# Performance work log

Measured on AMD Instinct MI355X. Metric: run time of the kernel, lower is better.

Reference implementation:

```python
import jax, jax.numpy as jnp
import numpy as np

N, T, H, O, S, R = 64, 1024, 256, 80, 128, 2


def _lin(k, fin, fout):
    kw, kb = jax.random.split(k)
    s = 1.0 / np.sqrt(fin)
    return (jax.random.uniform(kw, (fout, fin), jnp.float32, -s, s),
            jax.random.uniform(kb, (fout,), jnp.float32, -s, s))


def _gru_params(k, fin, hid):
    k1, k2, k3, k4 = jax.random.split(k, 4)
    s = 1.0 / np.sqrt(hid)
    u = lambda kk, shp: jax.random.uniform(kk, shp, jnp.float32, -s, s)
    return u(k1, (3 * hid, fin)), u(k2, (3 * hid, hid)), u(k3, (3 * hid,)), u(k4, (3 * hid,))


def setup_inputs() -> dict:
    key = jax.random.key(0)
    ks = jax.random.split(key, 16)
    inp = {}
    inp["input_enc"] = jax.random.normal(ks[0], (N, T, 2 * H), jnp.float32)
    inp["input_attW_enc"] = jax.random.normal(ks[1], (N, T, 2 * H), jnp.float32)
    inp["input_dec"] = jax.random.normal(ks[2], (N, O), jnp.float32)
    inp["style_vec"] = jax.random.normal(ks[3], (N, 1, S), jnp.float32)
    lengths = jnp.sort(jax.random.randint(ks[4], (N,), 1, T + 1))[::-1]
    inp["lengths_enc"] = lengths.at[0].set(T)  # pack_padded requires max(len)==T, descending
    inp["pw1"], inp["pb1"] = _lin(ks[5], O, 2 * H)
    inp["pw2"], inp["pb2"] = _lin(ks[6], 2 * H, H)
    inp["wdec"], inp["bdec"] = _lin(ks[7], 2 * H, 2 * H)
    inp["ga_ih"], inp["ga_hh"], inp["ga_bih"], inp["ga_bhh"] = _gru_params(ks[8], 3 * H + S, 2 * H)
    inp["wattn"], inp["battn"] = _lin(ks[9], 2 * H, 1)
    inp["wsc"], inp["bsc"] = _lin(ks[10], 4 * H + S, 2 * H)
    inp["g1_ih"], inp["g1_hh"], inp["g1_bih"], inp["g1_bhh"] = _gru_params(ks[11], 4 * H + S, 2 * H)
    inp["g2_ih"], inp["g2_hh"], inp["g2_bih"], inp["g2_bhh"] = _gru_params(ks[12], 2 * H, 2 * H)
    inp["wout"], inp["bout"] = _lin(ks[13], 2 * H, R * O)
    return inp


def _gru_cell(x, h, w_ih, w_hh, b_ih, b_hh):
    # PyTorch GRU cell: gates order (r, z, n)
    gi = x @ w_ih.T + b_ih
    gh = h @ w_hh.T + b_hh
    ir, iz, inn = jnp.split(gi, 3, -1)
    hr, hz, hn = jnp.split(gh, 3, -1)
    r = jax.nn.sigmoid(ir + hr)
    z = jax.nn.sigmoid(iz + hz)
    n = jnp.tanh(inn + r * hn)
    return (1.0 - z) * n + z * h


def reference(input_enc, input_attW_enc, input_dec, style_vec,
              pw1, pb1, pw2, pb2, wdec, bdec,
              ga_ih, ga_hh, ga_bih, ga_bhh,
              wattn, battn, wsc, bsc,
              g1_ih, g1_hh, g1_bih, g1_bhh,
              g2_ih, g2_hh, g2_bih, g2_bhh,
              wout, bout, lengths_enc):
    Nn, Tt, D2 = input_enc.shape
    Hh = D2 // 2
    # prenet (dropout disabled: eval-mode reference)
    pre = jax.nn.relu(jax.nn.relu(input_dec @ pw1.T + pb1) @ pw2.T + pb2)  # (N,H)
    ctx0 = jnp.zeros((Nn, 2 * Hh), input_enc.dtype)  # input_context=None -> zeros
    sv = style_vec[:, 0, :]
    x_att = jnp.concatenate([pre, ctx0, sv], axis=-1)  # (N,3H+S)
    h0 = jnp.zeros((Nn, 2 * Hh), input_enc.dtype)  # hidden states start None -> zeros
    out_att = _gru_cell(x_att, h0, ga_ih, ga_hh, ga_bih, ga_bhh)  # (N,2H)
    attW_dec = out_att @ wdec.T + bdec  # (N,2H), broadcast over T (expand_as)
    e = jnp.tanh(input_attW_enc + attW_dec[:, None, :])  # (N,T,2H)
    score = e @ wattn.T + battn  # (N,T,1)
    mask = (jnp.arange(Tt)[None, :] < lengths_enc[:, None]).astype(score.dtype)[..., None]
    w = jnp.exp(score) * mask  # pack/pad zeroes padded positions
    w = w / jnp.maximum(jnp.sum(w, axis=1, keepdims=True), 1e-12)  # F.normalize(p=1, dim=1)
    attn_applied = jnp.einsum('nt,ntd->nd', w[..., 0], input_enc)  # bmm(w^T, enc) -> (N,2H)
    out_dec = jnp.concatenate([attn_applied, out_att, sv], axis=-1)  # (N,4H+S)
    residual = out_dec @ wsc.T + bsc
    h1 = _gru_cell(out_dec, h0, g1_ih, g1_hh, g1_bih, g1_bhh)
    residual = residual + h1
    h2 = _gru_cell(residual, h0, g2_ih, g2_hh, g2_bih, g2_bhh)
    residual = residual + h2
    output = (residual @ wout.T + bout).reshape(Nn, R, -1)  # (N,r,O)
    return output, attn_applied[:, None, :]
```

## Files before the change

### kernel.cpp

```cpp
#include <hip/hip_runtime.h>
#include <math.h>

#define NB  64
#define TT  1024
#define H2  512
#define SS  128
#define OO  80
#define FIN_A 896
#define FIN_1 1152
#define CH  32

__device__ __forceinline__ float fast_rcp(float x) { return __builtin_amdgcn_rcpf(x); }
__device__ __forceinline__ float fast_sigmoid(float x) { return fast_rcp(1.0f + __expf(-x)); }
__device__ __forceinline__ float fast_tanh(float x) {
    float e = __expf(2.0f * x);
    return 1.0f - 2.0f * fast_rcp(e + 1.0f);
}
__device__ __forceinline__ float wred(float p) {
    #pragma unroll
    for (int o = 32; o > 0; o >>= 1) p += __shfl_xor(p, o, 64);
    return p;
}

__global__ void k_l1(const float* __restrict__ xdec, const float* __restrict__ pw1,
                     const float* __restrict__ pb1, const float* __restrict__ sv,
                     float* __restrict__ t1T, float* __restrict__ xaT,
                     float* __restrict__ out_decT) {
    int wv = threadIdx.x >> 6, lane = threadIdx.x & 63;
    if (blockIdx.x < 128) {
        int i = blockIdx.x * 4 + wv;
        const float* w = pw1 + i * OO;
        const float* x = xdec + lane * OO;
        float acc = 0.0f;
        #pragma unroll 8
        for (int k = 0; k < OO; ++k) acc += w[k] * x[k];
        t1T[i * 64 + lane] = fmaxf(acc + pb1[i], 0.0f);
    } else {
        int s = (blockIdx.x - 128) * 4 + wv;
        float v = sv[lane * SS + s];
        xaT[(256 + s) * 64 + lane] = v;
        out_decT[(1024 + s) * 64 + lane] = v;
    }
}

__global__ void k_l2(const float* __restrict__ t1T, const float* __restrict__ pw2,
                     const float* __restrict__ pb2, float* __restrict__ xaT) {
    int i = blockIdx.x;
    int wv = threadIdx.x >> 6, lane = threadIdx.x & 63;
    int k0 = wv * 128;
    const float* w = pw2 + (size_t)i * H2 + k0;
    const float* xT = t1T + k0 * 64;
    float p = 0.0f;
    #pragma unroll 8
    for (int k = 0; k < 128; ++k) p += w[k] * xT[k * 64 + lane];
    __shared__ float s[4][64];
    s[wv][lane] = p;
    __syncthreads();
    if (wv == 0) {
        float acc = s[0][lane] + s[1][lane] + s[2][lane] + s[3][lane];
        xaT[i * 64 + lane] = fmaxf(acc + pb2[i], 0.0f);
    }
}

__global__ void k_gruA(const float* __restrict__ xaT, const float* __restrict__ ga_ih,
                       const float* __restrict__ ga_bih, const float* __restrict__ ga_bhh,
                       float* __restrict__ out_decT) {
    int j = blockIdx.x;
    int wv = threadIdx.x >> 6, lane = threadIdx.x & 63;
    int k0 = wv * 96;
    const float* wr = ga_ih + (size_t)j * FIN_A;
    const float* wz = ga_ih + (size_t)(H2 + j) * FIN_A;
    const float* wn = ga_ih + (size_t)(2 * H2 + j) * FIN_A;
    float pr = 0.0f, pz = 0.0f, pn = 0.0f;
    #pragma unroll 8
    for (int kk = 0; kk < 96; ++kk) {
        int k = k0 + kk;
        int wc = k + (k >= 256 ? 512 : 0);
        float xv = xaT[k * 64 + lane];
        pr += wr[wc] * xv; pz += wz[wc] * xv; pn += wn[wc] * xv;
    }
    __shared__ float s[3][4][64];
    s[0][wv][lane] = pr; s[1][wv][lane] = pz; s[2][wv][lane] = pn;
    __syncthreads();
    if (wv == 0) {
        float fr = s[0][0][lane] + s[0][1][lane] + s[0][2][lane] + s[0][3][lane];
        float fz = s[1][0][lane] + s[1][1][lane] + s[1][2][lane] + s[1][3][lane];
        float fn = s[2][0][lane] + s[2][1][lane] + s[2][2][lane] + s[2][3][lane];
        float r = fast_sigmoid(fr + ga_bih[j] + ga_bhh[j]);
        float z = fast_sigmoid(fz + ga_bih[H2 + j] + ga_bhh[H2 + j]);
        float nn = fast_tanh(fn + ga_bih[2 * H2 + j] + r * ga_bhh[2 * H2 + j]);
        out_decT[(H2 + j) * 64 + lane] = (1.0f - z) * nn;
    }
}

__global__ void k_attw(const float* __restrict__ out_decT, const float* __restrict__ wdec,
                       const float* __restrict__ bdec, float* __restrict__ attW_dec) {
    int i = blockIdx.x;
    int wv = threadIdx.x >> 6, lane = threadIdx.x & 63;
    int k0 = wv * 128;
    const float* w = wdec + (size_t)i * H2 + k0;
    const float* xT = out_decT + (H2 + k0) * 64;
    float p = 0.0f;
    #pragma unroll 8
    for (int k = 0; k < 128; ++k) p += w[k] * xT[k * 64 + lane];
    __shared__ float s[4][64];
    s[wv][lane] = p;
    __syncthreads();
    if (wv == 0) {
        float acc = s[0][lane] + s[1][lane] + s[2][lane] + s[3][lane];
        attW_dec[lane * H2 + i] = acc + bdec[i];
    }
}

__global__ void k_score(const float* __restrict__ attw_enc, const float* __restrict__ attW_dec,
                        const float* __restrict__ wattn, const float* __restrict__ battn,
                        const int* __restrict__ lengths, float* __restrict__ ew) {
    int wv = threadIdx.x >> 6, lane = threadIdx.x & 63;
    int row = blockIdx.x * 4 + wv;
    int n = row >> 10, t = row & 1023;
    if (t >= lengths[n]) { if (lane == 0) ew[row] = 0.0f; return; }
    const float4* e4 = (const float4*)(attw_enc + (size_t)row * H2);
    const float4* d4 = (const float4*)(attW_dec + n * H2);
    const float4* w4 = (const float4*)wattn;
    float p = 0.0f;
    #pragma unroll
    for (int m = 0; m < 2; ++m) {
        int idx = lane + m * 64;
        float4 e = e4[idx], d = d4[idx], w = w4[idx];
        p += fast_tanh(e.x + d.x) * w.x + fast_tanh(e.y + d.y) * w.y +
             fast_tanh(e.z + d.z) * w.z + fast_tanh(e.w + d.w) * w.w;
    }
    p = wred(p);
    if (lane == 0) ew[row] = __expf(p + battn[0]);
}

__global__ void k_apply(const float* __restrict__ enc, const float* __restrict__ ew,
                        float* __restrict__ num_part ,
                        float* __restrict__ den_part ) {
    int n = blockIdx.y, c = blockIdx.x;
    int wv = threadIdx.x >> 6, lane = threadIdx.x & 63;
    int t0 = c * (TT / CH) + wv * (TT / CH / 4);
    int d0 = lane * 8;
    const float* base = enc + ((size_t)n * TT + t0) * H2 + d0;
    const float* ewp = ew + n * TT + t0;
    float4 a0 = {0, 0, 0, 0}, a1 = {0, 0, 0, 0};
    float dp = 0.0f;
    #pragma unroll
    for (int t = 0; t < TT / CH / 4; ++t) {
        float wt = ewp[t];
        if (wt != 0.0f) {
            const float4* v4 = (const float4*)(base + (size_t)t * H2);
            float4 v0 = v4[0], v1 = v4[1];
            a0.x += wt * v0.x; a0.y += wt * v0.y; a0.z += wt * v0.z; a0.w += wt * v0.w;
            a1.x += wt * v1.x; a1.y += wt * v1.y; a1.z += wt * v1.z; a1.w += wt * v1.w;
            dp += wt;
        }
    }
    __shared__ float s[4 * 512];
    __shared__ float sd[4];
    float4* srow = (float4*)(s + wv * 512 + d0);
    srow[0] = a0; srow[1] = a1;
    if (lane == 0) sd[wv] = dp;
    __syncthreads();
    int d = threadIdx.x;
    float r0 = s[d] + s[512 + d] + s[1024 + d] + s[1536 + d];
    float r1 = s[256 + d] + s[768 + d] + s[1280 + d] + s[1792 + d];
    num_part[((size_t)c * H2 + d) * 64 + n] = r0;
    num_part[((size_t)c * H2 + 256 + d) * 64 + n] = r1;
    if (threadIdx.x == 0) den_part[c * NB + n] = sd[0] + sd[1] + sd[2] + sd[3];
}

__global__ void k_reduce(const float* __restrict__ num_part, const float* __restrict__ den_part,
                         float* __restrict__ out, float* __restrict__ out_decT) {
    int d = blockIdx.x * 4 + (threadIdx.x >> 6);
    int lane = threadIdx.x & 63;
    float s = 0.0f, den = 0.0f;
    #pragma unroll 8
    for (int c = 0; c < CH; ++c) {
        s += num_part[((size_t)c * H2 + d) * 64 + lane];
        den += den_part[c * NB + lane];
    }
    float a = s / fmaxf(den, 1e-12f);
    out_decT[d * 64 + lane] = a;
    out[NB * 160 + lane * H2 + d] = a;
}

__global__ void k_sc_h1(const float* __restrict__ out_decT, const float* __restrict__ wsc,
                        const float* __restrict__ bsc, const float* __restrict__ g1_ih,
                        const float* __restrict__ g1_bih, const float* __restrict__ g1_bhh,
                        float* __restrict__ res1T) {
    int j = blockIdx.x;
    int wv = threadIdx.x >> 6, lane = threadIdx.x & 63;
    int k0 = wv * 288;
    const float* ws_ = wsc + (size_t)j * FIN_1 + k0;
    const float* wr = g1_ih + (size_t)j * FIN_1 + k0;
    const float* wz = g1_ih + (size_t)(H2 + j) * FIN_1 + k0;
    const float* wn = g1_ih + (size_t)(2 * H2 + j) * FIN_1 + k0;
    const float* xT = out_decT + k0 * 64;
    float ps = 0.0f, pr = 0.0f, pz = 0.0f, pn = 0.0f;
    #pragma unroll 8
    for (int k = 0; k < 288; ++k) {
        float xv = xT[k * 64 + lane];
        ps += ws_[k] * xv; pr += wr[k] * xv; pz += wz[k] * xv; pn += wn[k] * xv;
    }
    __shared__ float s[4][4][64];
    s[0][wv][lane] = ps; s[1][wv][lane] = pr; s[2][wv][lane] = pz; s[3][wv][lane] = pn;
    __syncthreads();
    if (wv == 0) {
        float fs = s[0][0][lane] + s[0][1][lane] + s[0][2][lane] + s[0][3][lane];
        float fr = s[1][0][lane] + s[1][1][lane] + s[1][2][lane] + s[1][3][lane];
        float fz = s[2][0][lane] + s[2][1][lane] + s[2][2][lane] + s[2][3][lane];
        float fn = s[3][0][lane] + s[3][1][lane] + s[3][2][lane] + s[3][3][lane];
        float r = fast_sigmoid(fr + g1_bih[j] + g1_bhh[j]);
        float z = fast_sigmoid(fz + g1_bih[H2 + j] + g1_bhh[H2 + j]);
        float nn = fast_tanh(fn + g1_bih[2 * H2 + j] + r * g1_bhh[2 * H2 + j]);
        res1T[j * 64 + lane] = fs + bsc[j] + (1.0f - z) * nn;
    }
}

__global__ void k_h2(const float* __restrict__ res1T, const float* __restrict__ g2_ih,
                     const float* __restrict__ g2_bih, const float* __restrict__ g2_bhh,
                     float* __restrict__ res2T) {
    int j = blockIdx.x;
    int wv = threadIdx.x >> 6, lane = threadIdx.x & 63;
    int k0 = wv * 128;
    const float* wr = g2_ih + (size_t)j * H2 + k0;
    const float* wz = g2_ih + (size_t)(H2 + j) * H2 + k0;
    const float* wn = g2_ih + (size_t)(2 * H2 + j) * H2 + k0;
    const float* xT = res1T + k0 * 64;
    float pr = 0.0f, pz = 0.0f, pn = 0.0f;
    #pragma unroll 8
    for (int k = 0; k < 128; ++k) {
        float xv = xT[k * 64 + lane];
        pr += wr[k] * xv; pz += wz[k] * xv; pn += wn[k] * xv;
    }
    __shared__ float s[3][4][64];
    s[0][wv][lane] = pr; s[1][wv][lane] = pz; s[2][wv][lane] = pn;
    __syncthreads();
    if (wv == 0) {
        float fr = s[0][0][lane] + s[0][1][lane] + s[0][2][lane] + s[0][3][lane];
        float fz = s[1][0][lane] + s[1][1][lane] + s[1][2][lane] + s[1][3][lane];
        float fn = s[2][0][lane] + s[2][1][lane] + s[2][2][lane] + s[2][3][lane];
        float r = fast_sigmoid(fr + g2_bih[j] + g2_bhh[j]);
        float z = fast_sigmoid(fz + g2_bih[H2 + j] + g2_bhh[H2 + j]);
        float nn = fast_tanh(fn + g2_bih[2 * H2 + j] + r * g2_bhh[2 * H2 + j]);
        res2T[j * 64 + lane] = res1T[j * 64 + lane] + (1.0f - z) * nn;
    }
}

__global__ void k_out(const float* __restrict__ res2T, const float* __restrict__ wout,
                      const float* __restrict__ bout, float* __restrict__ out) {
    int i = blockIdx.x;
    int wv = threadIdx.x >> 6, lane = threadIdx.x & 63;
    int k0 = wv * 128;
    const float* w = wout + (size_t)i * H2 + k0;
    const float* xT = res2T + k0 * 64;
    float p = 0.0f;
    #pragma unroll 8
    for (int k = 0; k < 128; ++k) p += w[k] * xT[k * 64 + lane];
    __shared__ float s[4][64];
    s[wv][lane] = p;
    __syncthreads();
    if (wv == 0) {
        float acc = s[0][lane] + s[1][lane] + s[2][lane] + s[3][lane];
        out[lane * 160 + i] = acc + bout[i];
    }
}

extern "C" void kernel_launch(void* const* d_in, const int* in_sizes, int n_in,
                              void* d_out, int out_size, void* d_ws, size_t ws_size,
                              hipStream_t stream) {
    const float* input_enc      = (const float*)d_in[0];
    const float* input_attW_enc = (const float*)d_in[1];
    const float* input_dec      = (const float*)d_in[2];
    const float* style_vec      = (const float*)d_in[3];
    const int*   lengths_enc    = (const int*)d_in[4];
    const float* pw1  = (const float*)d_in[5];
    const float* pb1  = (const float*)d_in[6];
    const float* pw2  = (const float*)d_in[7];
    const float* pb2  = (const float*)d_in[8];
    const float* wdec = (const float*)d_in[9];
    const float* bdec = (const float*)d_in[10];
    const float* ga_ih  = (const float*)d_in[11];
    const float* ga_bih = (const float*)d_in[13];
    const float* ga_bhh = (const float*)d_in[14];
    const float* wattn  = (const float*)d_in[15];
    const float* battn  = (const float*)d_in[16];
    const float* wsc    = (const float*)d_in[17];
    const float* bsc    = (const float*)d_in[18];
    const float* g1_ih  = (const float*)d_in[19];
    const float* g1_bih = (const float*)d_in[21];
    const float* g1_bhh = (const float*)d_in[22];
    const float* g2_ih  = (const float*)d_in[23];
    const float* g2_bih = (const float*)d_in[25];
    const float* g2_bhh = (const float*)d_in[26];
    const float* wout   = (const float*)d_in[27];
    const float* bout   = (const float*)d_in[28];
    float* out = (float*)d_out;

    float* ws = (float*)d_ws;
    float* num_part = ws;
    float* den_part = ws + 1048576;
    float* t1T      = ws + 1050624;
    float* xaT      = ws + 1083392;
    float* out_decT = ws + 1107968;
    float* attW_dec = ws + 1181696;
    float* ew       = ws + 1214464;
    float* res1T    = ws + 1280000;
    float* res2T    = ws + 1312768;

    k_l1<<<160, 256, 0, stream>>>(input_dec, pw1, pb1, style_vec, t1T, xaT, out_decT);
    k_l2<<<256, 256, 0, stream>>>(t1T, pw2, pb2, xaT);
    k_gruA<<<512, 256, 0, stream>>>(xaT, ga_ih, ga_bih, ga_bhh, out_decT);
    k_attw<<<512, 256, 0, stream>>>(out_decT, wdec, bdec, attW_dec);
    k_score<<<NB * TT / 4, 256, 0, stream>>>(input_attW_enc, attW_dec, wattn, battn,
                                             lengths_enc, ew);
    k_apply<<<dim3(CH, NB), 256, 0, stream>>>(input_enc, ew, num_part, den_part);
    k_reduce<<<128, 256, 0, stream>>>(num_part, den_part, out, out_decT);
    k_sc_h1<<<512, 256, 0, stream>>>(out_decT, wsc, bsc, g1_ih, g1_bih, g1_bhh, res1T);
    k_h2<<<512, 256, 0, stream>>>(res1T, g2_ih, g2_bih, g2_bhh, res2T);
    k_out<<<160, 256, 0, stream>>>(res2T, wout, bout, out);
}
```

Baseline: 401.1 us.

## Fuse attention score into apply kernel and widen GEMV blocks to eight waves

Merges the score kernel into the attention-apply kernel. Each block computes exp-scores for its 32 timesteps into shared memory before the weighted sum, so the global ew buffer and one launch go away. It also doubles the waves per block in the small GEMV/GRU kernels so the K dimension is split eight ways, and k_sc_h1 uses float2 weight loads. The risk is that the fused kernel serialises score and apply work inside each block, with less parallelism in the score phase than the old 16K-block launch.

```diff
diff --git a/kernel.cpp b/kernel.cpp
--- a/kernel.cpp
+++ b/kernel.cpp
@@ -43,49 +43,55 @@
     }
 }
 
-__global__ void k_l2(const float* __restrict__ t1T, const float* __restrict__ pw2,
-                     const float* __restrict__ pb2, float* __restrict__ xaT) {
+__global__ __launch_bounds__(512) void k_l2(const float* __restrict__ t1T,
+                                            const float* __restrict__ pw2,
+                                            const float* __restrict__ pb2,
+                                            float* __restrict__ xaT) {
     int i = blockIdx.x;
     int wv = threadIdx.x >> 6, lane = threadIdx.x & 63;
-    int k0 = wv * 128;
+    int k0 = wv * 64;
     const float* w = pw2 + (size_t)i * H2 + k0;
     const float* xT = t1T + k0 * 64;
     float p = 0.0f;
     #pragma unroll 8
-    for (int k = 0; k < 128; ++k) p += w[k] * xT[k * 64 + lane];
-    __shared__ float s[4][64];
+    for (int k = 0; k < 64; ++k) p += w[k] * xT[k * 64 + lane];
+    __shared__ float s[8][64];
     s[wv][lane] = p;
     __syncthreads();
     if (wv == 0) {
-        float acc = s[0][lane] + s[1][lane] + s[2][lane] + s[3][lane];
+        float acc = 0.0f;
+        #pragma unroll
+        for (int q = 0; q < 8; ++q) acc += s[q][lane];
         xaT[i * 64 + lane] = fmaxf(acc + pb2[i], 0.0f);
     }
 }
 
-__global__ void k_gruA(const float* __restrict__ xaT, const float* __restrict__ ga_ih,
-                       const float* __restrict__ ga_bih, const float* __restrict__ ga_bhh,
-                       float* __restrict__ out_decT) {
+__global__ __launch_bounds__(512) void k_gruA(const float* __restrict__ xaT,
+                                              const float* __restrict__ ga_ih,
+                                              const float* __restrict__ ga_bih,
+                                              const float* __restrict__ ga_bhh,
+                                              float* __restrict__ out_decT) {
     int j = blockIdx.x;
     int wv = threadIdx.x >> 6, lane = threadIdx.x & 63;
-    int k0 = wv * 96;
+    int k0 = wv * 48;
     const float* wr = ga_ih + (size_t)j * FIN_A;
     const float* wz = ga_ih + (size_t)(H2 + j) * FIN_A;
     const float* wn = ga_ih + (size_t)(2 * H2 + j) * FIN_A;
     float pr = 0.0f, pz = 0.0f, pn = 0.0f;
     #pragma unroll 8
-    for (int kk = 0; kk < 96; ++kk) {
+    for (int kk = 0; kk < 48; ++kk) {
         int k = k0 + kk;
         int wc = k + (k >= 256 ? 512 : 0);
         float xv = xaT[k * 64 + lane];
         pr += wr[wc] * xv; pz += wz[wc] * xv; pn += wn[wc] * xv;
     }
-    __shared__ float s[3][4][64];
+    __shared__ float s[3][8][64];
     s[0][wv][lane] = pr; s[1][wv][lane] = pz; s[2][wv][lane] = pn;
     __syncthreads();
     if (wv == 0) {
-        float fr = s[0][0][lane] + s[0][1][lane] + s[0][2][lane] + s[0][3][lane];
-        float fz = s[1][0][lane] + s[1][1][lane] + s[1][2][lane] + s[1][3][lane];
-        float fn = s[2][0][lane] + s[2][1][lane] + s[2][2][lane] + s[2][3][lane];
+        float fr = 0.0f, fz = 0.0f, fn = 0.0f;
+        #pragma unroll
+        for (int q = 0; q < 8; ++q) { fr += s[0][q][lane]; fz += s[1][q][lane]; fn += s[2][q][lane]; }
         float r = fast_sigmoid(fr + ga_bih[j] + ga_bhh[j]);
         float z = fast_sigmoid(fz + ga_bih[H2 + j] + ga_bhh[H2 + j]);
         float nn = fast_tanh(fn + ga_bih[2 * H2 + j] + r * ga_bhh[2 * H2 + j]);
@@ -93,71 +99,84 @@
     }
 }
 
-__global__ void k_attw(const float* __restrict__ out_decT, const float* __restrict__ wdec,
-                       const float* __restrict__ bdec, float* __restrict__ attW_dec) {
+__global__ __launch_bounds__(512) void k_attw(const float* __restrict__ out_decT,
+                                              const float* __restrict__ wdec,
+                                              const float* __restrict__ bdec,
+                                              float* __restrict__ attW_dec) {
     int i = blockIdx.x;
     int wv = threadIdx.x >> 6, lane = threadIdx.x & 63;
-    int k0 = wv * 128;
+    int k0 = wv * 64;
     const float* w = wdec + (size_t)i * H2 + k0;
     const float* xT = out_decT + (H2 + k0) * 64;
     float p = 0.0f;
     #pragma unroll 8
-    for (int k = 0; k < 128; ++k) p += w[k] * xT[k * 64 + lane];
-    __shared__ float s[4][64];
+    for (int k = 0; k < 64; ++k) p += w[k] * xT[k * 64 + lane];
+    __shared__ float s[8][64];
     s[wv][lane] = p;
     __syncthreads();
     if (wv == 0) {
-        float acc = s[0][lane] + s[1][lane] + s[2][lane] + s[3][lane];
+        float acc = 0.0f;
+        #pragma unroll
+        for (int q = 0; q < 8; ++q) acc += s[q][lane];
         attW_dec[lane * H2 + i] = acc + bdec[i];
     }
 }
 
-__global__ void k_score(const float* __restrict__ attw_enc, const float* __restrict__ attW_dec,
-                        const float* __restrict__ wattn, const float* __restrict__ battn,
-                        const int* __restrict__ lengths, float* __restrict__ ew) {
-    int wv = threadIdx.x >> 6, lane = threadIdx.x & 63;
-    int row = blockIdx.x * 4 + wv;
-    int n = row >> 10, t = row & 1023;
-    if (t >= lengths[n]) { if (lane == 0) ew[row] = 0.0f; return; }
-    const float4* e4 = (const float4*)(attw_enc + (size_t)row * H2);
-    const float4* d4 = (const float4*)(attW_dec + n * H2);
-    const float4* w4 = (const float4*)wattn;
-    float p = 0.0f;
-    #pragma unroll
-    for (int m = 0; m < 2; ++m) {
-        int idx = lane + m * 64;
-        float4 e = e4[idx], d = d4[idx], w = w4[idx];
-        p += fast_tanh(e.x + d.x) * w.x + fast_tanh(e.y + d.y) * w.y +
-             fast_tanh(e.z + d.z) * w.z + fast_tanh(e.w + d.w) * w.w;
-    }
-    p = wred(p);
-    if (lane == 0) ew[row] = __expf(p + battn[0]);
-}
-
-__global__ void k_apply(const float* __restrict__ enc, const float* __restrict__ ew,
-                        float* __restrict__ num_part ,
-                        float* __restrict__ den_part ) {
+__global__ __launch_bounds__(256, 8) void k_attn(
+        const float* __restrict__ enc, const float* __restrict__ attw_enc,
+        const float* __restrict__ attW_dec, const float* __restrict__ wattn,
+        const float* __restrict__ battn, const int* __restrict__ lengths,
+        float* __restrict__ num_part ,
+        float* __restrict__ den_part ) {
     int n = blockIdx.y, c = blockIdx.x;
     int wv = threadIdx.x >> 6, lane = threadIdx.x & 63;
-    int t0 = c * (TT / CH) + wv * (TT / CH / 4);
+    int t0 = c * (TT / CH);
+    int len = lengths[n];
+    __shared__ float sew[TT / CH];
+    __shared__ float s[4 * 512];
+    __shared__ float sd[4];
+
+    {
+        const float4* d4 = (const float4*)(attW_dec + n * H2);
+        const float4* w4 = (const float4*)wattn;
+        float b = battn[0];
+        #pragma unroll
+        for (int r = 0; r < 8; ++r) {
+            int t = t0 + wv * 8 + r;
+            float val = 0.0f;
+            if (t < len) {
+                const float4* e4 = (const float4*)(attw_enc + ((size_t)(n * TT + t)) * H2);
+                float p = 0.0f;
+                #pragma unroll
+                for (int m = 0; m < 2; ++m) {
+                    int idx = lane + m * 64;
+                    float4 e = e4[idx], d = d4[idx], w = w4[idx];
+                    p += fast_tanh(e.x + d.x) * w.x + fast_tanh(e.y + d.y) * w.y +
+                         fast_tanh(e.z + d.z) * w.z + fast_tanh(e.w + d.w) * w.w;
+                }
+                p = wred(p);
+                val = __expf(p + b);
+            }
+            if (lane == 0) sew[wv * 8 + r] = val;
+        }
+    }
+    __syncthreads();
+
     int d0 = lane * 8;
-    const float* base = enc + ((size_t)n * TT + t0) * H2 + d0;
-    const float* ewp = ew + n * TT + t0;
+    const float* base = enc + ((size_t)(n * TT + t0 + wv * 8)) * H2 + d0;
     float4 a0 = {0, 0, 0, 0}, a1 = {0, 0, 0, 0};
     float dp = 0.0f;
     #pragma unroll
-    for (int t = 0; t < TT / CH / 4; ++t) {
-        float wt = ewp[t];
+    for (int r = 0; r < 8; ++r) {
+        float wt = sew[wv * 8 + r];
         if (wt != 0.0f) {
-            const float4* v4 = (const float4*)(base + (size_t)t * H2);
+            const float4* v4 = (const float4*)(base + (size_t)r * H2);
             float4 v0 = v4[0], v1 = v4[1];
             a0.x += wt * v0.x; a0.y += wt * v0.y; a0.z += wt * v0.z; a0.w += wt * v0.w;
             a1.x += wt * v1.x; a1.y += wt * v1.y; a1.z += wt * v1.z; a1.w += wt * v1.w;
             dp += wt;
         }
     }
-    __shared__ float s[4 * 512];
-    __shared__ float sd[4];
     float4* srow = (float4*)(s + wv * 512 + d0);
     srow[0] = a0; srow[1] = a1;
     if (lane == 0) sd[wv] = dp;
@@ -185,32 +204,46 @@
     out[NB * 160 + lane * H2 + d] = a;
 }
 
-__global__ void k_sc_h1(const float* __restrict__ out_decT, const float* __restrict__ wsc,
-                        const float* __restrict__ bsc, const float* __restrict__ g1_ih,
-                        const float* __restrict__ g1_bih, const float* __restrict__ g1_bhh,
-                        float* __restrict__ res1T) {
+__global__ __launch_bounds__(512) void k_sc_h1(const float* __restrict__ out_decT,
+                                               const float* __restrict__ wsc,
+                                               const float* __restrict__ bsc,
+                                               const float* __restrict__ g1_ih,
+                                               const float* __restrict__ g1_bih,
+                                               const float* __restrict__ g1_bhh,
+                                               float* __restrict__ res1T) {
     int j = blockIdx.x;
     int wv = threadIdx.x >> 6, lane = threadIdx.x & 63;
-    int k0 = wv * 288;
+    int k0 = wv * 144;
     const float* ws_ = wsc + (size_t)j * FIN_1 + k0;
     const float* wr = g1_ih + (size_t)j * FIN_1 + k0;
     const float* wz = g1_ih + (size_t)(H2 + j) * FIN_1 + k0;
     const float* wn = g1_ih + (size_t)(2 * H2 + j) * FIN_1 + k0;
     const float* xT = out_decT + k0 * 64;
-    float ps = 0.0f, pr = 0.0f, pz = 0.0f, pn = 0.0f;
-    #pragma unroll 8
-    for (int k = 0; k < 288; ++k) {
-        float xv = xT[k * 64 + lane];
-        ps += ws_[k] * xv; pr += wr[k] * xv; pz += wz[k] * xv; pn += wn[k] * xv;
-    }
-    __shared__ float s[4][4][64];
-    s[0][wv][lane] = ps; s[1][wv][lane] = pr; s[2][wv][lane] = pz; s[3][wv][lane] = pn;
-    __syncthreads();
-    if (wv == 0) {
-        float fs = s[0][0][lane] + s[0][1][lane] + s[0][2][lane] + s[0][3][lane];
-        float fr = s[1][0][lane] + s[1][1][lane] + s[1][2][lane] + s[1][3][lane];
-        float fz = s[2][0][lane] + s[2][1][lane] + s[2][2][lane] + s[2][3][lane];
-        float fn = s[3][0][lane] + s[3][1][lane] + s[3][2][lane] + s[3][3][lane];
+    float2 ps = {0, 0}, pr = {0, 0}, pz = {0, 0}, pn = {0, 0};
+    #pragma unroll 4
+    for (int k = 0; k < 144; k += 2) {
+        float x0 = xT[k * 64 + lane];
+        float x1 = xT[(k + 1) * 64 + lane];
+        float2 a = *(const float2*)(ws_ + k);
+        float2 b = *(const float2*)(wr + k);
+        float2 cc = *(const float2*)(wz + k);
+        float2 dd = *(const float2*)(wn + k);
+        ps.x += a.x * x0; ps.y += a.y * x1;
+        pr.x += b.x * x0; pr.y += b.y * x1;
+        pz.x += cc.x * x0; pz.y += cc.y * x1;
+        pn.x += dd.x * x0; pn.y += dd.y * x1;
+    }
+    __shared__ float s[4][8][64];
+    s[0][wv][lane] = ps.x + ps.y; s[1][wv][lane] = pr.x + pr.y;
+    s[2][wv][lane] = pz.x + pz.y; s[3][wv][lane] = pn.x + pn.y;
+    __syncthreads();
+    if (wv == 0) {
+        float fs = 0.0f, fr = 0.0f, fz = 0.0f, fn = 0.0f;
+        #pragma unroll
+        for (int q = 0; q < 8; ++q) {
+            fs += s[0][q][lane]; fr += s[1][q][lane];
+            fz += s[2][q][lane]; fn += s[3][q][lane];
+        }
         float r = fast_sigmoid(fr + g1_bih[j] + g1_bhh[j]);
         float z = fast_sigmoid(fz + g1_bih[H2 + j] + g1_bhh[H2 + j]);
         float nn = fast_tanh(fn + g1_bih[2 * H2 + j] + r * g1_bhh[2 * H2 + j]);
@@ -218,29 +251,31 @@
     }
 }
 
-__global__ void k_h2(const float* __restrict__ res1T, const float* __restrict__ g2_ih,
-                     const float* __restrict__ g2_bih, const float* __restrict__ g2_bhh,
-                     float* __restrict__ res2T) {
+__global__ __launch_bounds__(512) void k_h2(const float* __restrict__ res1T,
+                                            const float* __restrict__ g2_ih,
+                                            const float* __restrict__ g2_bih,
+                                            const float* __restrict__ g2_bhh,
+                                            float* __restrict__ res2T) {
     int j = blockIdx.x;
     int wv = threadIdx.x >> 6, lane = threadIdx.x & 63;
-    int k0 = wv * 128;
+    int k0 = wv * 64;
     const float* wr = g2_ih + (size_t)j * H2 + k0;
     const float* wz = g2_ih + (size_t)(H2 + j) * H2 + k0;
     const float* wn = g2_ih + (size_t)(2 * H2 + j) * H2 + k0;
     const float* xT = res1T + k0 * 64;
     float pr = 0.0f, pz = 0.0f, pn = 0.0f;
     #pragma unroll 8
-    for (int k = 0; k < 128; ++k) {
+    for (int k = 0; k < 64; ++k) {
         float xv = xT[k * 64 + lane];
         pr += wr[k] * xv; pz += wz[k] * xv; pn += wn[k] * xv;
     }
-    __shared__ float s[3][4][64];
+    __shared__ float s[3][8][64];
     s[0][wv][lane] = pr; s[1][wv][lane] = pz; s[2][wv][lane] = pn;
     __syncthreads();
     if (wv == 0) {
-        float fr = s[0][0][lane] + s[0][1][lane] + s[0][2][lane] + s[0][3][lane];
-        float fz = s[1][0][lane] + s[1][1][lane] + s[1][2][lane] + s[1][3][lane];
-        float fn = s[2][0][lane] + s[2][1][lane] + s[2][2][lane] + s[2][3][lane];
+        float fr = 0.0f, fz = 0.0f, fn = 0.0f;
+        #pragma unroll
+        for (int q = 0; q < 8; ++q) { fr += s[0][q][lane]; fz += s[1][q][lane]; fn += s[2][q][lane]; }
         float r = fast_sigmoid(fr + g2_bih[j] + g2_bhh[j]);
         float z = fast_sigmoid(fz + g2_bih[H2 + j] + g2_bhh[H2 + j]);
         float nn = fast_tanh(fn + g2_bih[2 * H2 + j] + r * g2_bhh[2 * H2 + j]);
@@ -248,21 +283,25 @@
     }
 }
 
-__global__ void k_out(const float* __restrict__ res2T, const float* __restrict__ wout,
-                      const float* __restrict__ bout, float* __restrict__ out) {
+__global__ __launch_bounds__(512) void k_out(const float* __restrict__ res2T,
+                                             const float* __restrict__ wout,
+                                             const float* __restrict__ bout,
+                                             float* __restrict__ out) {
     int i = blockIdx.x;
     int wv = threadIdx.x >> 6, lane = threadIdx.x & 63;
-    int k0 = wv * 128;
+    int k0 = wv * 64;
     const float* w = wout + (size_t)i * H2 + k0;
     const float* xT = res2T + k0 * 64;
     float p = 0.0f;
     #pragma unroll 8
-    for (int k = 0; k < 128; ++k) p += w[k] * xT[k * 64 + lane];
-    __shared__ float s[4][64];
+    for (int k = 0; k < 64; ++k) p += w[k] * xT[k * 64 + lane];
+    __shared__ float s[8][64];
     s[wv][lane] = p;
     __syncthreads();
     if (wv == 0) {
-        float acc = s[0][lane] + s[1][lane] + s[2][lane] + s[3][lane];
+        float acc = 0.0f;
+        #pragma unroll
+        for (int q = 0; q < 8; ++q) acc += s[q][lane];
         out[lane * 160 + i] = acc + bout[i];
     }
 }
@@ -305,19 +344,17 @@
     float* xaT      = ws + 1083392;
     float* out_decT = ws + 1107968;
     float* attW_dec = ws + 1181696;
-    float* ew       = ws + 1214464;
-    float* res1T    = ws + 1280000;
-    float* res2T    = ws + 1312768;
+    float* res1T    = ws + 1214464;
+    float* res2T    = ws + 1247232;
 
     k_l1<<<160, 256, 0, stream>>>(input_dec, pw1, pb1, style_vec, t1T, xaT, out_decT);
-    k_l2<<<256, 256, 0, stream>>>(t1T, pw2, pb2, xaT);
-    k_gruA<<<512, 256, 0, stream>>>(xaT, ga_ih, ga_bih, ga_bhh, out_decT);
-    k_attw<<<512, 256, 0, stream>>>(out_decT, wdec, bdec, attW_dec);
-    k_score<<<NB * TT / 4, 256, 0, stream>>>(input_attW_enc, attW_dec, wattn, battn,
-                                             lengths_enc, ew);
-    k_apply<<<dim3(CH, NB), 256, 0, stream>>>(input_enc, ew, num_part, den_part);
+    k_l2<<<256, 512, 0, stream>>>(t1T, pw2, pb2, xaT);
+    k_gruA<<<512, 512, 0, stream>>>(xaT, ga_ih, ga_bih, ga_bhh, out_decT);
+    k_attw<<<512, 512, 0, stream>>>(out_decT, wdec, bdec, attW_dec);
+    k_attn<<<dim3(CH, NB), 256, 0, stream>>>(input_enc, input_attW_enc, attW_dec,
+                                             wattn, battn, lengths_enc, num_part, den_part);
     k_reduce<<<128, 256, 0, stream>>>(num_part, den_part, out, out_decT);
-    k_sc_h1<<<512, 256, 0, stream>>>(out_decT, wsc, bsc, g1_ih, g1_bih, g1_bhh, res1T);
-    k_h2<<<512, 256, 0, stream>>>(res1T, g2_ih, g2_bih, g2_bhh, res2T);
-    k_out<<<160, 256, 0, stream>>>(res2T, wout, bout, out);
-}
+    k_sc_h1<<<512, 512, 0, stream>>>(out_decT, wsc, bsc, g1_ih, g1_bih, g1_bhh, res1T);
+    k_h2<<<512, 512, 0, stream>>>(res1T, g2_ih, g2_bih, g2_bhh, res2T);
+    k_out<<<160, 512, 0, stream>>>(res2T, wout, bout, out);
+}
```

Result: faster. 388.4 us (-3.2%).
